# Optimization experiments

Measured on AMD Instinct MI355X. Metric: run time of the kernel, lower is better.

## Reference

```python
import jax, jax.numpy as jnp
import numpy as np

NUM_HEADS = 12
QK_SCALE = 1.0
V_SCALE = 1.0
TOPK = 8        # attn_inter_topk
BS_RATIO = 0.5  # ratio of reference samples to mini-batch size
EPS = 1e-6
NEG = jnp.float32(-1e30)


def rmsnorm(x, w):
    return x * jax.lax.rsqrt(jnp.mean(x * x, axis=-1, keepdims=True) + EPS) * w


def setup_inputs() -> dict:
    key = jax.random.key(0)
    k0, k1, k2, k3 = jax.random.split(key, 4)
    B, P, D = 32, 197, 768
    Pp = 49  # int(P * rep_tkn_ratio)
    return {
        "q": jax.random.normal(k0, (B, P, D), jnp.float32),
        "k": jax.random.normal(k1, (B, P, D), jnp.float32),
        "v": jax.random.normal(k2, (B, P, D), jnp.float32),
        "wq": jnp.ones((D,), jnp.float32),
        "wk": jnp.ones((D,), jnp.float32),
        "wv": jnp.ones((D,), jnp.float32),
        "random_tkn_idxs": jax.random.randint(k3, (Pp,), 0, P),
    }


def reference(q, k, v, wq, wk, wv, random_tkn_idxs):
    B, P, D = q.shape
    H = NUM_HEADS
    d = D // H
    Pp = random_tkn_idxs.shape[0]
    n = int(B * BS_RATIO)  # number of reference samples (same-device, across_gpus=False)

    # qk/v RMSNorm over full embedding dim, then head split -> (b, h, p, d)
    qn, kn, vn = rmsnorm(q, wq), rmsnorm(k, wk), rmsnorm(v, wv)
    split = lambda t: t.reshape(B, P, H, d).transpose(0, 2, 1, 3)
    qh, kh, vh = split(qn), split(kn), split(vn)

    # standard self-attention weights
    attn = jax.nn.softmax(
        jnp.einsum("bhid,bhjd->bhij", qh, kh) * (QK_SCALE * d ** -0.5), axis=-1
    )

    # representative tokens from the n reference samples: gather random tokens of v
    rep = vh[:n][:, :, random_tkn_idxs, :]  # (n, h, p', d)

    # inter-sample token similarity on values: (m, n, h, p, p')
    sim = jnp.einsum("mhid,nhjd->mnhij", vh, rep) * V_SCALE

    # exclude a sample's own tokens from its reference set (sample indices 0..n-1)
    self_mask = jnp.arange(B)[:, None] == jnp.arange(n)[None, :]  # (m, n)
    sim = jnp.where(self_mask[:, :, None, None, None], NEG, sim)

    # flatten reference axis -> (m, h, p, n*p'); keep only top-k, softmax over kept
    simf = sim.transpose(0, 2, 3, 1, 4).reshape(B, H, P, n * Pp)
    thr = jax.lax.top_k(simf, TOPK)[0][..., -1:]
    w = jax.nn.softmax(jnp.where(simf >= thr, simf, NEG), axis=-1)

    # aligned values gathered from reference tokens
    rep_flat = rep.transpose(1, 0, 2, 3).reshape(H, n * Pp, d)  # (h, n*p', d)
    v_aligned = jnp.einsum("mhpk,hkd->mhpd", w, rep_flat)

    out = jnp.einsum("bhij,bhjd->bhid", attn, vh + v_aligned)  # (b, h, p, d)
    return out.transpose(0, 2, 1, 3).reshape(B, P, D)
```

## Files before the change

kernel.cpp:

```cpp
#include <hip/hip_runtime.h>

#define B_    32
#define P_    197
#define D_    768
#define H_    12
#define DH    64
#define PP_   49
#define NREF  16
#define NP_   784
#define TOPK_ 8
#define EPS_  1e-6f
#define NEGF  -1e30f
#define SCALE 0.125f

#define IT    8
#define NIT   25
#define NJ    13

__device__ inline float waveReduceMax(float v) {
    #pragma unroll
    for (int off = 32; off; off >>= 1) v = fmaxf(v, __shfl_xor(v, off, 64));
    return v;
}
__device__ inline float waveReduceSum(float v) {
    #pragma unroll
    for (int off = 32; off; off >>= 1) v += __shfl_xor(v, off, 64);
    return v;
}
__device__ inline int waveReduceSumI(int v) {
    #pragma unroll
    for (int off = 32; off; off >>= 1) v += __shfl_xor(v, off, 64);
    return v;
}

__global__ __launch_bounds__(256) void rmsnorm_kernel(
    const float* __restrict__ x, const float* __restrict__ w,
    float* __restrict__ o) {
    int row = blockIdx.x;
    int t = threadIdx.x;
    const float* xr = x + (size_t)row * D_;
    float v0 = xr[t], v1 = xr[t + 256], v2 = xr[t + 512];
    float ss = v0 * v0 + v1 * v1 + v2 * v2;
    __shared__ float red[4];
    ss = waveReduceSum(ss);
    if ((t & 63) == 0) red[t >> 6] = ss;
    __syncthreads();
    float r = rsqrtf((red[0] + red[1] + red[2] + red[3]) * (1.0f / D_) + EPS_);
    float* orow = o + (size_t)row * D_;
    orow[t]       = v0 * r * w[t];
    orow[t + 256] = v1 * r * w[t + 256];
    orow[t + 512] = v2 * r * w[t + 512];
}

__global__ __launch_bounds__(256) void ktrans_kernel(
    const float* __restrict__ kn, float* __restrict__ knT) {
    __shared__ float tile[64][65];
    int bh = blockIdx.x;
    int h = bh % H_;
    int b = bh / H_;
    int t = threadIdx.x, lane = t & 63, wid = t >> 6;
    for (int j0 = 0; j0 < P_; j0 += 64) {
        __syncthreads();
        for (int r = wid; r < 64; r += 4) {
            int j = j0 + r;
            tile[r][lane] = (j < P_) ? kn[((size_t)(b * P_ + j)) * D_ + h * DH + lane] : 0.f;
        }
        __syncthreads();
        for (int r = wid; r < 64; r += 4) {
            int j = j0 + lane;
            if (j < P_) knT[((size_t)bh * DH + r) * P_ + j] = tile[lane][r];
        }
    }
}

__global__ __launch_bounds__(256) void rep_gather_kernel(
    const float* __restrict__ vn, const int* __restrict__ idx,
    float* __restrict__ repRM, float* __restrict__ repTG) {
    int u = blockIdx.x * 256 + threadIdx.x;
    if (u >= H_ * NP_ * DH) return;
    int dd  = u & 63;
    int col = (u >> 6) % NP_;
    int h   = u / (NP_ * DH);
    int nref = col / PP_;
    int jp   = col - nref * PP_;
    float val = vn[((size_t)(nref * P_ + idx[jp])) * D_ + h * DH + dd];
    repRM[u] = val;
    repTG[((size_t)(h * 16 + (dd >> 2)) * NP_ + col) * 4 + (dd & 3)] = val;
}

__global__ __launch_bounds__(256) void sim_topk_kernel(
    const float* __restrict__ vn, const float* __restrict__ repRM,
    const float* __restrict__ repTG, float* __restrict__ vsum) {
    __shared__ float  simS[IT][NP_ + 1];
    __shared__ float4 vrow4[IT][16];
    __shared__ int    keptIdx[IT][32];
    __shared__ int    keptCnt[IT];

    int bid = blockIdx.x;
    int it = bid % NIT;
    int h  = (bid / NIT) % H_;
    int m  = bid / (NIT * H_);
    int i0 = it * IT;
    int t = threadIdx.x, lane = t & 63, w = t >> 6;

    if (t < IT * 16) {
        int r = t >> 4, kk = t & 15;
        int i = i0 + r;
        float4 val = make_float4(0.f, 0.f, 0.f, 0.f);
        if (i < P_) val = *(const float4*)(vn + ((size_t)(m * P_ + i)) * D_ + h * DH + kk * 4);
        vrow4[r][kk] = val;
    }
    __syncthreads();

    int c0 = lane + 64 * (w + 0);
    int c1 = lane + 64 * (w + 4);
    int c2 = lane + 64 * (w + 8);
    int c3 = lane + 64 * (w + 12);
    int a0 = (c0 < NP_) ? c0 : NP_ - 1;
    int a1 = (c1 < NP_) ? c1 : NP_ - 1;
    int a2 = (c2 < NP_) ? c2 : NP_ - 1;
    int a3 = (c3 < NP_) ? c3 : NP_ - 1;

    const float4* rep4 = (const float4*)repTG + (size_t)h * 16 * NP_;

    float acc[IT][4];
    #pragma unroll
    for (int rr = 0; rr < IT; rr++)
        #pragma unroll
        for (int jj = 0; jj < 4; jj++) acc[rr][jj] = 0.f;

    #pragma unroll 2
    for (int kk = 0; kk < 16; kk++) {
        const float4* rk = rep4 + (size_t)kk * NP_;
        float4 r0 = rk[a0];
        float4 r1 = rk[a1];
        float4 r2 = rk[a2];
        float4 r3 = rk[a3];
        #pragma unroll
        for (int rr = 0; rr < IT; rr++) {
            float4 vv = vrow4[rr][kk];
            acc[rr][0] = fmaf(vv.x, r0.x, acc[rr][0]); acc[rr][0] = fmaf(vv.y, r0.y, acc[rr][0]);
            acc[rr][0] = fmaf(vv.z, r0.z, acc[rr][0]); acc[rr][0] = fmaf(vv.w, r0.w, acc[rr][0]);
            acc[rr][1] = fmaf(vv.x, r1.x, acc[rr][1]); acc[rr][1] = fmaf(vv.y, r1.y, acc[rr][1]);
            acc[rr][1] = fmaf(vv.z, r1.z, acc[rr][1]); acc[rr][1] = fmaf(vv.w, r1.w, acc[rr][1]);
            acc[rr][2] = fmaf(vv.x, r2.x, acc[rr][2]); acc[rr][2] = fmaf(vv.y, r2.y, acc[rr][2]);
            acc[rr][2] = fmaf(vv.z, r2.z, acc[rr][2]); acc[rr][2] = fmaf(vv.w, r2.w, acc[rr][2]);
            acc[rr][3] = fmaf(vv.x, r3.x, acc[rr][3]); acc[rr][3] = fmaf(vv.y, r3.y, acc[rr][3]);
            acc[rr][3] = fmaf(vv.z, r3.z, acc[rr][3]); acc[rr][3] = fmaf(vv.w, r3.w, acc[rr][3]);
        }
    }

    #pragma unroll
    for (int jj = 0; jj < 4; jj++) {
        int j = w + 4 * jj;
        int col = lane + 64 * j;
        if (j < NJ && col < NP_) {
            bool mk = (m < NREF) && (col / PP_ == m);
            #pragma unroll
            for (int rr = 0; rr < IT; rr++)
                simS[rr][col] = mk ? NEGF : acc[rr][jj];
        }
    }
    __syncthreads();

    const float* reph = repRM + (size_t)h * NP_ * DH;
    for (int rr = w; rr < IT; rr += 4) {
        int i = i0 + rr;
        if (i >= P_) continue;
        if (lane == 0) keptCnt[rr] = 0;
        float sv[NJ];
        #pragma unroll
        for (int j = 0; j < NJ; j++) {
            int c = lane + 64 * j;
            sv[j] = (c < NP_) ? simS[rr][c] : NEGF;
        }
        float thr = 3.0e38f, vmax = NEGF;
        int remaining = TOPK_;
        for (int iter = 0; iter < TOPK_; iter++) {
            float lm = NEGF;
            #pragma unroll
            for (int j = 0; j < NJ; j++) if (sv[j] < thr) lm = fmaxf(lm, sv[j]);
            float gm = waveReduceMax(lm);
            if (iter == 0) vmax = gm;
            int lc = 0;
            #pragma unroll
            for (int j = 0; j < NJ; j++) if (sv[j] == gm) lc++;
            int gc = waveReduceSumI(lc);
            thr = gm;
            if (gc >= remaining) break;
            remaining -= gc;
        }
        float lsum = 0.f;
        #pragma unroll
        for (int j = 0; j < NJ; j++) {
            if (sv[j] >= thr) {
                lsum += __expf(sv[j] - vmax);
                int slot = atomicAdd(&keptCnt[rr], 1);
                if (slot < 32) keptIdx[rr][slot] = lane + 64 * j;
            }
        }
        float Z = waveReduceSum(lsum);
        float invZ = 1.0f / Z;
        int nk = keptCnt[rr];
        if (nk > 32) nk = 32;
        float acc2 = 0.f;
        for (int z = 0; z < nk; z++) {
            int c = keptIdx[rr][z];
            float s = simS[rr][c];
            acc2 += __expf(s - vmax) * invZ * reph[(size_t)c * DH + lane];
        }
        vsum[((size_t)((m * H_ + h) * P_) + i) * DH + lane] =
            vn[((size_t)(m * P_ + i)) * D_ + h * DH + lane] + acc2;
    }
}

__global__ __launch_bounds__(256) void attn_kernel(
    const float* __restrict__ qn, const float* __restrict__ knT,
    const float* __restrict__ vsum, float* __restrict__ out) {
    __shared__ float4 qt4[IT][16];
    __shared__ float  sc[IT][256];
    __shared__ float  prowT[256][8];
    __shared__ float  redvA[IT][256];

    int bid = blockIdx.x;
    int it = bid % NIT;
    int h  = (bid / NIT) % H_;
    int b  = bid / (NIT * H_);
    int i0 = it * IT;
    int t = threadIdx.x, lane = t & 63, w = t >> 6;

    if (t < IT * 16) {
        int r = t >> 4, z = t & 15;
        int i = i0 + r;
        float4 val = make_float4(0.f, 0.f, 0.f, 0.f);
        if (i < P_) val = *(const float4*)(qn + ((size_t)(b * P_ + i)) * D_ + h * DH + z * 4);
        qt4[r][z] = val;
    }
    __syncthreads();

    {
        const float* kTb = knT + (size_t)(b * H_ + h) * DH * P_;
        int j = t;
        int jc = (j < P_) ? j : 0;
        float acc[IT];
        #pragma unroll
        for (int r = 0; r < IT; r++) acc[r] = 0.f;
        for (int z = 0; z < 16; z++) {
            const float* kp = kTb + (size_t)(4 * z) * P_ + jc;
            float k0 = kp[0 * P_], k1 = kp[1 * P_], k2 = kp[2 * P_], k3 = kp[3 * P_];
            #pragma unroll
            for (int r = 0; r < IT; r++) {
                float4 qv = qt4[r][z];
                acc[r] = fmaf(qv.x, k0, fmaf(qv.y, k1, fmaf(qv.z, k2, fmaf(qv.w, k3, acc[r]))));
            }
        }
        #pragma unroll
        for (int r = 0; r < IT; r++) sc[r][j] = acc[r] * SCALE;
    }
    __syncthreads();

    for (int rr = w; rr < IT; rr += 4) {
        float s0[4];
        #pragma unroll
        for (int g = 0; g < 4; g++) {
            int j = lane + 64 * g;
            s0[g] = (j < P_) ? sc[rr][j] : NEGF;
        }
        float mx = fmaxf(fmaxf(s0[0], s0[1]), fmaxf(s0[2], s0[3]));
        mx = waveReduceMax(mx);
        float e[4], ls = 0.f;
        #pragma unroll
        for (int g = 0; g < 4; g++) {
            int j = lane + 64 * g;
            e[g] = (j < P_) ? __expf(s0[g] - mx) : 0.f;
            ls += e[g];
        }
        float Z = waveReduceSum(ls);
        float invZ = 1.0f / Z;
        #pragma unroll
        for (int g = 0; g < 4; g++) prowT[lane + 64 * g][rr] = e[g] * invZ;
    }
    __syncthreads();

    {
        int dd = t & 63, q4 = t >> 6;
        const float* vb = vsum + (size_t)((b * H_ + h) * P_) * DH;
        float acc[IT];
        #pragma unroll
        for (int r = 0; r < IT; r++) acc[r] = 0.f;
        for (int jj = q4; jj < P_; jj += 4) {
            float vv = vb[(size_t)jj * DH + dd];
            float4 p0 = *(const float4*)&prowT[jj][0];
            float4 p1 = *(const float4*)&prowT[jj][4];
            acc[0] = fmaf(p0.x, vv, acc[0]);
            acc[1] = fmaf(p0.y, vv, acc[1]);
            acc[2] = fmaf(p0.z, vv, acc[2]);
            acc[3] = fmaf(p0.w, vv, acc[3]);
            acc[4] = fmaf(p1.x, vv, acc[4]);
            acc[5] = fmaf(p1.y, vv, acc[5]);
            acc[6] = fmaf(p1.z, vv, acc[6]);
            acc[7] = fmaf(p1.w, vv, acc[7]);
        }
        #pragma unroll
        for (int r = 0; r < IT; r++) redvA[r][q4 * 64 + dd] = acc[r];
    }
    __syncthreads();
    if (t < DH) {
        #pragma unroll
        for (int r = 0; r < IT; r++) {
            int i = i0 + r;
            if (i < P_) {
                float o = redvA[r][t] + redvA[r][64 + t] + redvA[r][128 + t] + redvA[r][192 + t];
                out[((size_t)(b * P_ + i)) * D_ + h * DH + t] = o;
            }
        }
    }
}

extern "C" void kernel_launch(void* const* d_in, const int* in_sizes, int n_in,
                              void* d_out, int out_size, void* d_ws, size_t ws_size,
                              hipStream_t stream) {
    const float* q  = (const float*)d_in[0];
    const float* k  = (const float*)d_in[1];
    const float* v  = (const float*)d_in[2];
    const float* wq = (const float*)d_in[3];
    const float* wk = (const float*)d_in[4];
    const float* wv = (const float*)d_in[5];
    const int* idx = (const int*)d_in[6];
    float* out = (float*)d_out;

    const size_t NTOK = (size_t)B_ * P_ * D_;
    const size_t REPSZ = (size_t)H_ * NP_ * DH;

    float* p = (float*)d_ws;
    float* qn    = p;  p += NTOK;
    float* kn    = p;  p += NTOK;
    float* knT   = p;  p += NTOK;
    float* repRM = p;  p += REPSZ;
    float* repTG = p;  p += REPSZ;
    float* vsum  = p;  p += NTOK;
    float* vn    = out;

    rmsnorm_kernel<<<B_ * P_, 256, 0, stream>>>(q, wq, qn);
    rmsnorm_kernel<<<B_ * P_, 256, 0, stream>>>(k, wk, kn);
    rmsnorm_kernel<<<B_ * P_, 256, 0, stream>>>(v, wv, vn);
    ktrans_kernel<<<B_ * H_, 256, 0, stream>>>(kn, knT);
    rep_gather_kernel<<<(H_ * NP_ * DH + 255) / 256, 256, 0, stream>>>(vn, idx, repRM, repTG);
    sim_topk_kernel<<<B_ * H_ * NIT, 256, 0, stream>>>(vn, repRM, repTG, vsum);
    attn_kernel<<<B_ * H_ * NIT, 256, 0, stream>>>(qn, knT, vsum, out);
}
```

Baseline: 521.1 us.

## Fuse three RMSNorms, drop K transpose, and trim padded sim columns

Merges the three RMSNorm launches into one grid, removes the K-transpose kernel and its workspace buffer so attention reads kn rows directly as float4, and cuts sim_topk's fourth column group so that only wave 0 handles the last 16 columns. This removes a full read-and-write pass over K, two launches, and the redundant clamped loads and FMAs for out-of-range columns. In exchange, each attention thread now reads its own 256-byte strided row of K instead of a coalesced transposed layout, and sim_topk has a divergent branch where only wave 0 works.

```diff
diff --git a/kernel.cpp b/kernel.cpp
--- a/kernel.cpp
+++ b/kernel.cpp
@@ -16,6 +16,7 @@
 #define IT    8
 #define NIT   25
 #define NJ    13
+#define NROW  (B_ * P_)
 
 __device__ inline float waveReduceMax(float v) {
     #pragma unroll
@@ -33,10 +34,17 @@
     return v;
 }
 
-__global__ __launch_bounds__(256) void rmsnorm_kernel(
-    const float* __restrict__ x, const float* __restrict__ w,
-    float* __restrict__ o) {
-    int row = blockIdx.x;
+__global__ __launch_bounds__(256) void rmsnorm3_kernel(
+    const float* __restrict__ q, const float* __restrict__ k,
+    const float* __restrict__ v, const float* __restrict__ wq,
+    const float* __restrict__ wk, const float* __restrict__ wv,
+    float* __restrict__ qn, float* __restrict__ kn, float* __restrict__ vn) {
+    int bid = blockIdx.x;
+    int which = bid / NROW;
+    int row = bid - which * NROW;
+    const float* x = (which == 0) ? q : (which == 1) ? k : v;
+    const float* w = (which == 0) ? wq : (which == 1) ? wk : wv;
+    float* o       = (which == 0) ? qn : (which == 1) ? kn : vn;
     int t = threadIdx.x;
     const float* xr = x + (size_t)row * D_;
     float v0 = xr[t], v1 = xr[t + 256], v2 = xr[t + 512];
@@ -50,27 +58,6 @@
     orow[t]       = v0 * r * w[t];
     orow[t + 256] = v1 * r * w[t + 256];
     orow[t + 512] = v2 * r * w[t + 512];
-}
-
-__global__ __launch_bounds__(256) void ktrans_kernel(
-    const float* __restrict__ kn, float* __restrict__ knT) {
-    __shared__ float tile[64][65];
-    int bh = blockIdx.x;
-    int h = bh % H_;
-    int b = bh / H_;
-    int t = threadIdx.x, lane = t & 63, wid = t >> 6;
-    for (int j0 = 0; j0 < P_; j0 += 64) {
-        __syncthreads();
-        for (int r = wid; r < 64; r += 4) {
-            int j = j0 + r;
-            tile[r][lane] = (j < P_) ? kn[((size_t)(b * P_ + j)) * D_ + h * DH + lane] : 0.f;
-        }
-        __syncthreads();
-        for (int r = wid; r < 64; r += 4) {
-            int j = j0 + lane;
-            if (j < P_) knT[((size_t)bh * DH + r) * P_ + j] = tile[lane][r];
-        }
-    }
 }
 
 __global__ __launch_bounds__(256) void rep_gather_kernel(
@@ -112,22 +99,20 @@
     }
     __syncthreads();
 
-    int c0 = lane + 64 * (w + 0);
-    int c1 = lane + 64 * (w + 4);
-    int c2 = lane + 64 * (w + 8);
-    int c3 = lane + 64 * (w + 12);
-    int a0 = (c0 < NP_) ? c0 : NP_ - 1;
-    int a1 = (c1 < NP_) ? c1 : NP_ - 1;
-    int a2 = (c2 < NP_) ? c2 : NP_ - 1;
+    int a0 = lane + 64 * (w + 0);
+    int a1 = lane + 64 * (w + 4);
+    int a2 = lane + 64 * (w + 8);
+    int c3 = lane + 768;
     int a3 = (c3 < NP_) ? c3 : NP_ - 1;
 
     const float4* rep4 = (const float4*)repTG + (size_t)h * 16 * NP_;
 
-    float acc[IT][4];
-    #pragma unroll
-    for (int rr = 0; rr < IT; rr++)
-        #pragma unroll
-        for (int jj = 0; jj < 4; jj++) acc[rr][jj] = 0.f;
+    float acc[IT][3];
+    float accD[IT];
+    #pragma unroll
+    for (int rr = 0; rr < IT; rr++) {
+        acc[rr][0] = 0.f; acc[rr][1] = 0.f; acc[rr][2] = 0.f; accD[rr] = 0.f;
+    }
 
     #pragma unroll 2
     for (int kk = 0; kk < 16; kk++) {
@@ -135,7 +120,6 @@
         float4 r0 = rk[a0];
         float4 r1 = rk[a1];
         float4 r2 = rk[a2];
-        float4 r3 = rk[a3];
         #pragma unroll
         for (int rr = 0; rr < IT; rr++) {
             float4 vv = vrow4[rr][kk];
@@ -145,21 +129,31 @@
             acc[rr][1] = fmaf(vv.z, r1.z, acc[rr][1]); acc[rr][1] = fmaf(vv.w, r1.w, acc[rr][1]);
             acc[rr][2] = fmaf(vv.x, r2.x, acc[rr][2]); acc[rr][2] = fmaf(vv.y, r2.y, acc[rr][2]);
             acc[rr][2] = fmaf(vv.z, r2.z, acc[rr][2]); acc[rr][2] = fmaf(vv.w, r2.w, acc[rr][2]);
-            acc[rr][3] = fmaf(vv.x, r3.x, acc[rr][3]); acc[rr][3] = fmaf(vv.y, r3.y, acc[rr][3]);
-            acc[rr][3] = fmaf(vv.z, r3.z, acc[rr][3]); acc[rr][3] = fmaf(vv.w, r3.w, acc[rr][3]);
-        }
-    }
-
-    #pragma unroll
-    for (int jj = 0; jj < 4; jj++) {
-        int j = w + 4 * jj;
-        int col = lane + 64 * j;
-        if (j < NJ && col < NP_) {
-            bool mk = (m < NREF) && (col / PP_ == m);
+        }
+        if (w == 0) {
+            float4 r3 = rk[a3];
             #pragma unroll
-            for (int rr = 0; rr < IT; rr++)
-                simS[rr][col] = mk ? NEGF : acc[rr][jj];
-        }
+            for (int rr = 0; rr < IT; rr++) {
+                float4 vv = vrow4[rr][kk];
+                accD[rr] = fmaf(vv.x, r3.x, accD[rr]); accD[rr] = fmaf(vv.y, r3.y, accD[rr]);
+                accD[rr] = fmaf(vv.z, r3.z, accD[rr]); accD[rr] = fmaf(vv.w, r3.w, accD[rr]);
+            }
+        }
+    }
+
+    #pragma unroll
+    for (int jj = 0; jj < 3; jj++) {
+        int col = lane + 64 * (jj * 4 + w);
+        bool mk = (m < NREF) && (col / PP_ == m);
+        #pragma unroll
+        for (int rr = 0; rr < IT; rr++)
+            simS[rr][col] = mk ? NEGF : acc[rr][jj];
+    }
+    if (w == 0 && c3 < NP_) {
+        bool mk = (m < NREF) && (c3 / PP_ == m);
+        #pragma unroll
+        for (int rr = 0; rr < IT; rr++)
+            simS[rr][c3] = mk ? NEGF : accD[rr];
     }
     __syncthreads();
 
@@ -215,7 +209,7 @@
 }
 
 __global__ __launch_bounds__(256) void attn_kernel(
-    const float* __restrict__ qn, const float* __restrict__ knT,
+    const float* __restrict__ qn, const float* __restrict__ kn,
     const float* __restrict__ vsum, float* __restrict__ out) {
     __shared__ float4 qt4[IT][16];
     __shared__ float  sc[IT][256];
@@ -239,19 +233,20 @@
     __syncthreads();
 
     {
-        const float* kTb = knT + (size_t)(b * H_ + h) * DH * P_;
         int j = t;
         int jc = (j < P_) ? j : 0;
+        const float4* krow = (const float4*)(kn + ((size_t)(b * P_ + jc)) * D_ + h * DH);
         float acc[IT];
         #pragma unroll
         for (int r = 0; r < IT; r++) acc[r] = 0.f;
+        #pragma unroll 4
         for (int z = 0; z < 16; z++) {
-            const float* kp = kTb + (size_t)(4 * z) * P_ + jc;
-            float k0 = kp[0 * P_], k1 = kp[1 * P_], k2 = kp[2 * P_], k3 = kp[3 * P_];
+            float4 kv = krow[z];
             #pragma unroll
             for (int r = 0; r < IT; r++) {
                 float4 qv = qt4[r][z];
-                acc[r] = fmaf(qv.x, k0, fmaf(qv.y, k1, fmaf(qv.z, k2, fmaf(qv.w, k3, acc[r]))));
+                acc[r] = fmaf(qv.x, kv.x, fmaf(qv.y, kv.y,
+                         fmaf(qv.z, kv.z, fmaf(qv.w, kv.w, acc[r]))));
             }
         }
         #pragma unroll
@@ -335,17 +330,13 @@
     float* p = (float*)d_ws;
     float* qn    = p;  p += NTOK;
     float* kn    = p;  p += NTOK;
-    float* knT   = p;  p += NTOK;
     float* repRM = p;  p += REPSZ;
     float* repTG = p;  p += REPSZ;
     float* vsum  = p;  p += NTOK;
     float* vn    = out;
 
-    rmsnorm_kernel<<<B_ * P_, 256, 0, stream>>>(q, wq, qn);
-    rmsnorm_kernel<<<B_ * P_, 256, 0, stream>>>(k, wk, kn);
-    rmsnorm_kernel<<<B_ * P_, 256, 0, stream>>>(v, wv, vn);
-    ktrans_kernel<<<B_ * H_, 256, 0, stream>>>(kn, knT);
+    rmsnorm3_kernel<<<3 * NROW, 256, 0, stream>>>(q, k, v, wq, wk, wv, qn, kn, vn);
     rep_gather_kernel<<<(H_ * NP_ * DH + 255) / 256, 256, 0, stream>>>(vn, idx, repRM, repTG);
     sim_topk_kernel<<<B_ * H_ * NIT, 256, 0, stream>>>(vn, repRM, repTG, vsum);
-    attn_kernel<<<B_ * H_ * NIT, 256, 0, stream>>>(qn, knT, vsum, out);
-}
+    attn_kernel<<<B_ * H_ * NIT, 256, 0, stream>>>(qn, kn, vsum, out);
+}
```

Result: slower. 596.4 us (+14.5%).
